# Optimization experiments

Measured on AMD Instinct MI355X. Metric: run time of the kernel, lower is better.

Reference implementation:

```python
import jax, jax.numpy as jnp
import numpy as np

N, LQ, DM = 8, 2500, 256
NH, NL, NP, NZ = 8, 4, 8, 4
DH = DM // NH
SPATIAL = np.array([[64, 176], [32, 88], [16, 44], [8, 22]], dtype=np.int32)
LEN_IN = int((SPATIAL[:, 0] * SPATIAL[:, 1]).sum())


def setup_inputs() -> dict:
    key = jax.random.key(0)
    ks = jax.random.split(key, 10)
    query = jax.random.normal(ks[0], (N, LQ, DM), dtype=jnp.float32)
    query_pos = jax.random.normal(ks[1], (N, LQ, DM), dtype=jnp.float32)
    reference_points = jax.random.uniform(ks[2], (N, LQ, NZ, 2), dtype=jnp.float32)
    input_flatten = jax.random.normal(ks[3], (N, LEN_IN, DM), dtype=jnp.float32)
    input_spatial_shapes = jnp.asarray(SPATIAL)
    lsi = np.concatenate([[0], np.cumsum(SPATIAL[:, 0] * SPATIAL[:, 1])[:-1]]).astype(np.int32)
    input_level_start_index = jnp.asarray(lsi)
    # learned params (Linear: y = x @ W + b, W is (in, out))
    Wv = jax.random.normal(ks[4], (DM, DM), dtype=jnp.float32) * (1.0 / np.sqrt(DM))
    bv = jnp.zeros((DM,), dtype=jnp.float32)
    Wo = jax.random.normal(ks[5], (DM, NH * NL * NP * 2), dtype=jnp.float32) * 0.02
    bo = jax.random.normal(ks[6], (NH * NL * NP * 2,), dtype=jnp.float32) * 1.0
    Wa = jax.random.normal(ks[7], (DM, NH * NL * NP), dtype=jnp.float32) * 0.02
    ba = jnp.zeros((NH * NL * NP,), dtype=jnp.float32)
    return {"query": query, "query_pos": query_pos, "reference_points": reference_points,
            "input_flatten": input_flatten, "input_spatial_shapes": input_spatial_shapes,
            "input_level_start_index": input_level_start_index,
            "Wv": Wv, "bv": bv, "Wo": Wo, "bo": bo, "Wa": Wa, "ba": ba}


def _sample_level(v, h, w, loc):
    """Bilinear sample (grid_sample, align_corners=False, zero padding).
    v:   (N, h*w, NH, DH) level feature map
    loc: (N, Lq, NH, P, 2) normalized locations in [0,1] (x, y)
    returns (N, NH, Lq, P, DH)
    """
    n, hw, nh, dh = v.shape
    lq, p = loc.shape[1], loc.shape[3]
    x = loc[..., 0] * w - 0.5
    y = loc[..., 1] * h - 0.5
    x0f = jnp.floor(x)
    y0f = jnp.floor(y)
    wx = x - x0f
    wy = y - y0f
    x0 = x0f.astype(jnp.int32)
    y0 = y0f.astype(jnp.int32)
    vt = v.transpose(0, 2, 1, 3).reshape(n * nh, hw, dh)

    def gather(xi, yi, wgt):
        valid = ((xi >= 0) & (xi < w) & (yi >= 0) & (yi < h)).astype(v.dtype)
        idx = jnp.clip(yi, 0, h - 1) * w + jnp.clip(xi, 0, w - 1)  # (N,Lq,NH,P)
        idx = idx.transpose(0, 2, 1, 3).reshape(n * nh, lq * p)
        g = jnp.take_along_axis(vt, idx[:, :, None], axis=1)  # (N*NH, Lq*P, DH)
        wv = (wgt * valid).transpose(0, 2, 1, 3).reshape(n * nh, lq * p)
        return g * wv[:, :, None]

    out = (gather(x0, y0, (1 - wx) * (1 - wy))
           + gather(x0 + 1, y0, wx * (1 - wy))
           + gather(x0, y0 + 1, (1 - wx) * wy)
           + gather(x0 + 1, y0 + 1, wx * wy))
    return out.reshape(n, nh, lq, p, dh)


def _forward(query, query_pos, reference_points, input_flatten, spatial, Wv, bv, Wo, bo, Wa, ba):
    n, lq, _ = query.shape
    len_in = input_flatten.shape[1]
    # projections
    value = (input_flatten @ Wv + bv).reshape(n, len_in, NH, DH)
    off = (query @ Wo + bo).reshape(n, lq, NH, NL, NP, 2)
    aw = jax.nn.softmax((query @ Wa + ba).reshape(n, lq, NH, NL * NP), axis=-1)
    aw = aw.reshape(n, lq, NH, NL, NP)
    # normalize offsets by (W_l, H_l), add to Z-anchor reference points
    norm = jnp.asarray(np.stack([spatial[:, 1], spatial[:, 0]], -1), dtype=query.dtype)  # (NL,2)
    off = off / norm[None, None, None, :, None, :]
    off = off.reshape(n, lq, NH, NL, NP // NZ, NZ, 2)
    ref = reference_points[:, :, None, None, None, :, :]  # (N,Lq,1,1,1,NZ,2)
    loc = (ref + off).reshape(n, lq, NH, NL, NP, 2)
    # multi-scale deformable sampling + weighted reduction
    out = jnp.zeros((n, lq, NH, DH), dtype=query.dtype)
    start = 0
    for lvl in range(NL):
        h, w = int(spatial[lvl, 0]), int(spatial[lvl, 1])
        v_l = value[:, start:start + h * w]
        start += h * w
        samp = _sample_level(v_l, h, w, loc[:, :, :, lvl])  # (N,NH,Lq,NP,DH)
        out = out + jnp.einsum('nhqpd,nqhp->nqhd', samp, aw[:, :, :, lvl])
    return out.reshape(n, lq, DM)


def reference(query, query_pos, reference_points, input_flatten, input_spatial_shapes,
              input_level_start_index, Wv, bv, Wo, bo, Wa, ba):
    spatial = np.asarray(jax.device_get(input_spatial_shapes))
    return _forward(query, query_pos, reference_points, input_flatten, spatial,
                    Wv, bv, Wo, bo, Wa, ba)
```

## Files before the change

kernel.cpp:

```cpp
#include <hip/hip_runtime.h>
#include <hip/hip_fp16.h>

#define N_BATCH 8
#define LQ_     2500
#define DM_     256
#define NH_     8
#define NL_     4
#define NP_     8
#define DH_     32
#define LEN_IN_ 14960
#define KDIM    256

__constant__ int c_w[4]     = {176, 88, 44, 22};
__constant__ int c_h[4]     = {64, 32, 16, 8};
__constant__ int c_start[4] = {0, 11264, 14080, 14784};

using bf16x8 = __attribute__((ext_vector_type(8))) short;
using f32x4  = __attribute__((ext_vector_type(4))) float;

static __device__ inline void split_bf16(float v, unsigned short& hi, unsigned short& lo) {
    unsigned int u = __float_as_uint(v);
    hi = (unsigned short)(u >> 16);
    float hif = __uint_as_float(u & 0xFFFF0000u);
    float l = v - hif;
    lo = (unsigned short)(__float_as_uint(l) >> 16);
}

static __device__ inline unsigned short f2bf_rne(float v) {
    unsigned int u = __float_as_uint(v);
    u += 0x7FFFu + ((u >> 16) & 1u);
    return (unsigned short)(u >> 16);
}

__global__ __launch_bounds__(256) void conv_weights(
    const float* __restrict__ Wv, const float* __restrict__ Wo,
    const float* __restrict__ Wa, const float* __restrict__ bo,
    const float* __restrict__ ba,
    unsigned short* __restrict__ Wv_hi, unsigned short* __restrict__ Wv_lo,
    unsigned short* __restrict__ Wc_hi, unsigned short* __restrict__ Wc_lo,
    float* __restrict__ bcomb)
{
    int id = blockIdx.x * 256 + threadIdx.x;
    if (id < 256 * 256) {
        int n = id >> 8, k = id & 255;
        unsigned short h, l;
        split_bf16(Wv[k * 256 + n], h, l);
        Wv_hi[id] = h; Wv_lo[id] = l;
    } else {
        int id2 = id - 65536;
        if (id2 < 768 * 256) {
            int n = id2 >> 8, k = id2 & 255;
            float v = (n < 512) ? Wo[k * 512 + n] : Wa[k * 256 + (n - 512)];
            unsigned short h, l;
            split_bf16(v, h, l);
            Wc_hi[id2] = h; Wc_lo[id2] = l;
        }
    }
    if (id < 768) bcomb[id] = (id < 512) ? bo[id] : ba[id - 512];
}

template <bool BF16_OUT>
__global__ __launch_bounds__(512, 4) void gemm_mfma2(
    const float* __restrict__ A,
    const unsigned short* __restrict__ Bt_hi,
    const unsigned short* __restrict__ Bt_lo,
    const float* __restrict__ bias,
    float* __restrict__ C,
    unsigned short* __restrict__ Cb,
    int M, int N)
{
    __shared__ unsigned short As[128][40];
    __shared__ unsigned short Bh[128][40];
    __shared__ unsigned short Bl[128][40];

    const int tid  = threadIdx.x;
    const int ntn  = N >> 7;
    const int by   = blockIdx.x / ntn;
    const int bx   = blockIdx.x % ntn;
    const int row0 = by << 7, col0 = bx << 7;
    const int lane = tid & 63, wave = tid >> 6;
    const int wrow = (wave & 1) << 6, wcol = (wave >> 1) << 5;
    const int r16  = lane & 15, quad = lane >> 4;

    const int ar0 = tid >> 3;
    const int ac4 = (tid & 7) << 2;
    const int bn  = tid >> 2;
    const int bg  = (tid & 3) << 3;

    float4 pa[2];
    uint4  pbh, pbl;

#pragma unroll
    for (int i = 0; i < 2; ++i) {
        int row = row0 + ar0 + (i << 6);
        pa[i] = (row < M) ? *(const float4*)&A[(size_t)row * KDIM + ac4]
                          : make_float4(0.f, 0.f, 0.f, 0.f);
    }
    {
        size_t goff = (size_t)(col0 + bn) * KDIM + bg;
        pbh = *(const uint4*)&Bt_hi[goff];
        pbl = *(const uint4*)&Bt_lo[goff];
    }

    f32x4 acc[4][2];
#pragma unroll
    for (int i = 0; i < 4; ++i)
#pragma unroll
        for (int j = 0; j < 2; ++j) acc[i][j] = (f32x4){0.f, 0.f, 0.f, 0.f};

#pragma unroll
    for (int kt = 0; kt < KDIM; kt += 32) {
#pragma unroll
        for (int i = 0; i < 2; ++i) {
            int r = ar0 + (i << 6);
            ushort4 hv;
            hv.x = f2bf_rne(pa[i].x);
            hv.y = f2bf_rne(pa[i].y);
            hv.z = f2bf_rne(pa[i].z);
            hv.w = f2bf_rne(pa[i].w);
            *(ushort4*)&As[r][ac4] = hv;
        }
        *(uint4*)&Bh[bn][bg] = pbh;
        *(uint4*)&Bl[bn][bg] = pbl;
        __syncthreads();

        if (kt + 32 < KDIM) {
#pragma unroll
            for (int i = 0; i < 2; ++i) {
                int row = row0 + ar0 + (i << 6);
                pa[i] = (row < M)
                    ? *(const float4*)&A[(size_t)row * KDIM + kt + 32 + ac4]
                    : make_float4(0.f, 0.f, 0.f, 0.f);
            }
            size_t goff = (size_t)(col0 + bn) * KDIM + kt + 32 + bg;
            pbh = *(const uint4*)&Bt_hi[goff];
            pbl = *(const uint4*)&Bt_lo[goff];
        }

        bf16x8 fbh[2], fbl[2], fa[4];
#pragma unroll
        for (int tn = 0; tn < 2; ++tn) {
            int n = wcol + tn * 16 + r16;
            fbh[tn] = *(const bf16x8*)&Bh[n][quad << 3];
            fbl[tn] = *(const bf16x8*)&Bl[n][quad << 3];
        }
#pragma unroll
        for (int tm = 0; tm < 4; ++tm)
            fa[tm] = *(const bf16x8*)&As[wrow + tm * 16 + r16][quad << 3];
#pragma unroll
        for (int tm = 0; tm < 4; ++tm)
#pragma unroll
            for (int tn = 0; tn < 2; ++tn) {
                acc[tm][tn] = __builtin_amdgcn_mfma_f32_16x16x32_bf16(fa[tm], fbl[tn], acc[tm][tn], 0, 0, 0);
                acc[tm][tn] = __builtin_amdgcn_mfma_f32_16x16x32_bf16(fa[tm], fbh[tn], acc[tm][tn], 0, 0, 0);
            }
        __syncthreads();
    }

    float bvs[2];
#pragma unroll
    for (int tn = 0; tn < 2; ++tn) bvs[tn] = bias[col0 + wcol + tn * 16 + r16];
#pragma unroll
    for (int tm = 0; tm < 4; ++tm) {
#pragma unroll
        for (int i = 0; i < 4; ++i) {
            int row = row0 + wrow + tm * 16 + (quad << 2) + i;
            if (row < M) {
                if (!BF16_OUT) {
                    float* crow = C + (size_t)row * N + col0 + wcol + r16;
#pragma unroll
                    for (int tn = 0; tn < 2; ++tn)
                        crow[tn * 16] = acc[tm][tn][i] + bvs[tn];
                } else {
                    int n   = row / LEN_IN_;
                    int pix = row - n * LEN_IN_;
#pragma unroll
                    for (int tn = 0; tn < 2; ++tn) {
                        int col = col0 + wcol + tn * 16 + r16;
                        int h = col >> 5, dh = col & 31;
                        size_t addr = ((size_t)(n * NH_ + h) * LEN_IN_ + pix) * DH_ + dh;
                        Cb[addr] = f2bf_rne(acc[tm][tn][i] + bvs[tn]);
                    }
                }
            }
        }
    }
}

__global__ __launch_bounds__(256) void ms_sample(
    const unsigned short* __restrict__ value,
    const float* __restrict__ comb,
    const float* __restrict__ ref_pts,
    float* __restrict__ out)
{
    __shared__ uint4 s_desc[2048];

    const int bid = blockIdx.x;
    const int tid = threadIdx.x;

    {
        int q = tid >> 5, h = (tid >> 2) & 7, l = tid & 3;
        int nq = bid * 8 + q;
        const float* row = comb + (size_t)nq * 768;

        float4 L0 = *(const float4*)&row[512 + h * 32 + l * 8];
        float4 L1 = *(const float4*)&row[512 + h * 32 + l * 8 + 4];
        float lg[8] = {L0.x, L0.y, L0.z, L0.w, L1.x, L1.y, L1.z, L1.w};
        float m = lg[0];
#pragma unroll
        for (int i = 1; i < 8; ++i) m = fmaxf(m, lg[i]);
        m = fmaxf(m, __shfl_xor(m, 1));
        m = fmaxf(m, __shfl_xor(m, 2));
        float e[8], s = 0.f;
#pragma unroll
        for (int i = 0; i < 8; ++i) { e[i] = __expf(lg[i] - m); s += e[i]; }
        s += __shfl_xor(s, 1);
        s += __shfl_xor(s, 2);
        float inv = 1.f / s;

        float4 R0 = *(const float4*)&ref_pts[(size_t)nq * 8];
        float4 R1 = *(const float4*)&ref_pts[(size_t)nq * 8 + 4];
        float rx[4] = {R0.x, R0.z, R1.x, R1.z};
        float ry[4] = {R0.y, R0.w, R1.y, R1.w};

        float off[16];
#pragma unroll
        for (int i = 0; i < 4; ++i)
            *(float4*)&off[i * 4] = *(const float4*)&row[h * 64 + l * 16 + i * 4];

        float wl = (float)c_w[l], hl = (float)c_h[l];
        int wli = c_w[l], hli = c_h[l], st = c_start[l];
        uint4* dst = &s_desc[((q * 8 + h) * 4 + l) * 8];
#pragma unroll
        for (int p = 0; p < 8; ++p) {
            int z = p & 3;
            float a = e[p] * inv;
            float x = rx[z] * wl + off[p * 2 + 0] - 0.5f;
            float y = ry[z] * hl + off[p * 2 + 1] - 0.5f;
            float x0f = floorf(x), y0f = floorf(y);
            int   x0 = (int)x0f,  y0 = (int)y0f;
            float wx = x - x0f,   wy = y - y0f;
            unsigned short ix[4];
            float wt[4];
#pragma unroll
            for (int j = 0; j < 4; ++j) {
                int xi = x0 + (j & 1);
                int yi = y0 + (j >> 1);
                float w = ((j & 1) ? wx : 1.f - wx) * ((j >> 1) ? wy : 1.f - wy);
                bool valid = (xi >= 0) && (xi < wli) && (yi >= 0) && (yi < hli);
                int xc = min(max(xi, 0), wli - 1);
                int yc = min(max(yi, 0), hli - 1);
                ix[j] = (unsigned short)(st + yc * wli + xc);
                wt[j] = valid ? a * w : 0.f;
            }
            uint4 d;
            d.x = (unsigned int)ix[0] | ((unsigned int)ix[1] << 16);
            d.y = (unsigned int)ix[2] | ((unsigned int)ix[3] << 16);
            __half2 h01 = __floats2half2_rn(wt[0], wt[1]);
            __half2 h23 = __floats2half2_rn(wt[2], wt[3]);
            d.z = *(unsigned int*)&h01;
            d.w = *(unsigned int*)&h23;
            dst[p] = d;
        }
    }
    __syncthreads();

    int q = tid >> 5, h = (tid >> 2) & 7, dhg = tid & 3;
    int nq = bid * 8 + q;
    int n  = nq / LQ_;
    const unsigned short* vb = value
        + ((size_t)(n * NH_ + h) * LEN_IN_) * DH_ + dhg * 8;
    const uint4* desc = &s_desc[(q * 8 + h) * 32];

    float acc[8];
#pragma unroll
    for (int i = 0; i < 8; ++i) acc[i] = 0.f;

#pragma unroll 2
    for (int s = 0; s < 32; ++s) {
        uint4 d = desc[s];
        float2 w01 = __half22float2(*(const __half2*)&d.z);
        float2 w23 = __half22float2(*(const __half2*)&d.w);
        int i0 = d.x & 0xFFFF, i1 = d.x >> 16;
        int i2 = d.y & 0xFFFF, i3 = d.y >> 16;
        uint4 v0 = *(const uint4*)(vb + i0 * DH_);
        uint4 v1 = *(const uint4*)(vb + i1 * DH_);
        uint4 v2 = *(const uint4*)(vb + i2 * DH_);
        uint4 v3 = *(const uint4*)(vb + i3 * DH_);
        const uint4* vv[4] = {&v0, &v1, &v2, &v3};
        float ww[4] = {w01.x, w01.y, w23.x, w23.y};
#pragma unroll
        for (int c = 0; c < 4; ++c) {
            uint4 v = *vv[c];
            float w = ww[c];
            acc[0] = fmaf(__uint_as_float(v.x << 16), w, acc[0]);
            acc[1] = fmaf(__uint_as_float(v.x & 0xFFFF0000u), w, acc[1]);
            acc[2] = fmaf(__uint_as_float(v.y << 16), w, acc[2]);
            acc[3] = fmaf(__uint_as_float(v.y & 0xFFFF0000u), w, acc[3]);
            acc[4] = fmaf(__uint_as_float(v.z << 16), w, acc[4]);
            acc[5] = fmaf(__uint_as_float(v.z & 0xFFFF0000u), w, acc[5]);
            acc[6] = fmaf(__uint_as_float(v.w << 16), w, acc[6]);
            acc[7] = fmaf(__uint_as_float(v.w & 0xFFFF0000u), w, acc[7]);
        }
    }

    float* op = out + (size_t)nq * 256 + h * 32 + dhg * 8;
    *(float4*)&op[0] = make_float4(acc[0], acc[1], acc[2], acc[3]);
    *(float4*)&op[4] = make_float4(acc[4], acc[5], acc[6], acc[7]);
}

extern "C" void kernel_launch(void* const* d_in, const int* in_sizes, int n_in,
                              void* d_out, int out_size, void* d_ws, size_t ws_size,
                              hipStream_t stream)
{
    const float* query         = (const float*)d_in[0];
    const float* ref_pts       = (const float*)d_in[2];
    const float* input_flatten = (const float*)d_in[3];
    const float* Wv            = (const float*)d_in[6];
    const float* bv            = (const float*)d_in[7];
    const float* Wo            = (const float*)d_in[8];
    const float* bo            = (const float*)d_in[9];
    const float* Wa            = (const float*)d_in[10];
    const float* ba            = (const float*)d_in[11];
    float* out = (float*)d_out;

    char* ws = (char*)d_ws;
    size_t o = 0;
    unsigned short* Wv_hi = (unsigned short*)(ws + o); o += 256 * 256 * 2;
    unsigned short* Wv_lo = (unsigned short*)(ws + o); o += 256 * 256 * 2;
    unsigned short* Wc_hi = (unsigned short*)(ws + o); o += 768 * 256 * 2;
    unsigned short* Wc_lo = (unsigned short*)(ws + o); o += 768 * 256 * 2;
    float*          bcomb = (float*)(ws + o);          o += 768 * 4;
    o = (o + 511) & ~(size_t)511;
    unsigned short* value = (unsigned short*)(ws + o); o += (size_t)119680 * 256 * 2;
    o = (o + 511) & ~(size_t)511;
    float* combq = (float*)(ws + o); o += (size_t)20000 * 768 * 4;

    const int MV = N_BATCH * LEN_IN_;
    const int MQ = N_BATCH * LQ_;

    hipLaunchKernelGGL(conv_weights, dim3(1024), dim3(256), 0, stream,
                       Wv, Wo, Wa, bo, ba, Wv_hi, Wv_lo, Wc_hi, Wc_lo, bcomb);
    hipLaunchKernelGGL((gemm_mfma2<true>), dim3((MV / 128) * 2), dim3(512), 0, stream,
                       input_flatten, Wv_hi, Wv_lo, bv, (float*)nullptr, value, MV, 256);
    hipLaunchKernelGGL((gemm_mfma2<false>), dim3(((MQ + 127) / 128) * 6), dim3(512), 0, stream,
                       query, Wc_hi, Wc_lo, bcomb, combq, (unsigned short*)nullptr, MQ, 768);
    hipLaunchKernelGGL(ms_sample, dim3(MQ / 8), dim3(256), 0, stream,
                       value, combq, ref_pts, out);
}
```

Measured before the change: 402.6 us.

## Remap sampler and query GEMM blocks per XCD for value-slice L2 locality

The sampling kernel now assigns each block 64 queries of a single (batch, head) slice, and maps block IDs so that each XCD handles a fixed set of slices. The aim is to keep each slice's bf16 value map resident in that XCD's L2 rather than spread across all of them. The descriptor shared array is padded to 33 to avoid LDS bank conflicts. The combined query GEMM also gets an XCD-aware block swizzle with early exit for padding blocks, at the cost of some idle blocks and a partially filled tail chunk per slice.

```diff
diff --git a/kernel.cpp b/kernel.cpp
--- a/kernel.cpp
+++ b/kernel.cpp
@@ -59,7 +59,7 @@
     if (id < 768) bcomb[id] = (id < 512) ? bo[id] : ba[id - 512];
 }
 
-template <bool BF16_OUT>
+template <bool BF16_OUT, bool XSWIZ>
 __global__ __launch_bounds__(512, 4) void gemm_mfma2(
     const float* __restrict__ A,
     const unsigned short* __restrict__ Bt_hi,
@@ -67,7 +67,7 @@
     const float* __restrict__ bias,
     float* __restrict__ C,
     unsigned short* __restrict__ Cb,
-    int M, int N)
+    int M, int N, int nbm)
 {
     __shared__ unsigned short As[128][40];
     __shared__ unsigned short Bh[128][40];
@@ -75,8 +75,16 @@
 
     const int tid  = threadIdx.x;
     const int ntn  = N >> 7;
-    const int by   = blockIdx.x / ntn;
-    const int bx   = blockIdx.x % ntn;
+    int by, bx;
+    if (XSWIZ) {
+        int xcd = blockIdx.x & 7, j = blockIdx.x >> 3;
+        by = xcd + 8 * (j / ntn);
+        bx = j % ntn;
+        if (by >= nbm) return;
+    } else {
+        by = blockIdx.x / ntn;
+        bx = blockIdx.x % ntn;
+    }
     const int row0 = by << 7, col0 = bx << 7;
     const int lane = tid & 63, wave = tid >> 6;
     const int wrow = (wave & 1) << 6, wcol = (wave >> 1) << 5;
@@ -193,84 +201,92 @@
     const float* __restrict__ ref_pts,
     float* __restrict__ out)
 {
-    __shared__ uint4 s_desc[2048];
-
-    const int bid = blockIdx.x;
-    const int tid = threadIdx.x;
+    __shared__ uint4 s_desc[64][33];
+
+    const int b     = blockIdx.x;
+    const int xcd   = b & 7;
+    const int j     = b >> 3;
+    const int slice = (j / 40) * 8 + xcd;
+    const int chunk = j % 40;
+    const int n     = slice >> 3, h = slice & 7;
+    const int q0    = chunk * 64;
+    const int tid   = threadIdx.x;
 
     {
-        int q = tid >> 5, h = (tid >> 2) & 7, l = tid & 3;
-        int nq = bid * 8 + q;
-        const float* row = comb + (size_t)nq * 768;
-
-        float4 L0 = *(const float4*)&row[512 + h * 32 + l * 8];
-        float4 L1 = *(const float4*)&row[512 + h * 32 + l * 8 + 4];
-        float lg[8] = {L0.x, L0.y, L0.z, L0.w, L1.x, L1.y, L1.z, L1.w};
-        float m = lg[0];
-#pragma unroll
-        for (int i = 1; i < 8; ++i) m = fmaxf(m, lg[i]);
-        m = fmaxf(m, __shfl_xor(m, 1));
-        m = fmaxf(m, __shfl_xor(m, 2));
-        float e[8], s = 0.f;
-#pragma unroll
-        for (int i = 0; i < 8; ++i) { e[i] = __expf(lg[i] - m); s += e[i]; }
-        s += __shfl_xor(s, 1);
-        s += __shfl_xor(s, 2);
-        float inv = 1.f / s;
-
-        float4 R0 = *(const float4*)&ref_pts[(size_t)nq * 8];
-        float4 R1 = *(const float4*)&ref_pts[(size_t)nq * 8 + 4];
-        float rx[4] = {R0.x, R0.z, R1.x, R1.z};
-        float ry[4] = {R0.y, R0.w, R1.y, R1.w};
-
-        float off[16];
-#pragma unroll
-        for (int i = 0; i < 4; ++i)
-            *(float4*)&off[i * 4] = *(const float4*)&row[h * 64 + l * 16 + i * 4];
-
-        float wl = (float)c_w[l], hl = (float)c_h[l];
-        int wli = c_w[l], hli = c_h[l], st = c_start[l];
-        uint4* dst = &s_desc[((q * 8 + h) * 4 + l) * 8];
-#pragma unroll
-        for (int p = 0; p < 8; ++p) {
-            int z = p & 3;
-            float a = e[p] * inv;
-            float x = rx[z] * wl + off[p * 2 + 0] - 0.5f;
-            float y = ry[z] * hl + off[p * 2 + 1] - 0.5f;
-            float x0f = floorf(x), y0f = floorf(y);
-            int   x0 = (int)x0f,  y0 = (int)y0f;
-            float wx = x - x0f,   wy = y - y0f;
-            unsigned short ix[4];
-            float wt[4];
-#pragma unroll
-            for (int j = 0; j < 4; ++j) {
-                int xi = x0 + (j & 1);
-                int yi = y0 + (j >> 1);
-                float w = ((j & 1) ? wx : 1.f - wx) * ((j >> 1) ? wy : 1.f - wy);
-                bool valid = (xi >= 0) && (xi < wli) && (yi >= 0) && (yi < hli);
-                int xc = min(max(xi, 0), wli - 1);
-                int yc = min(max(yi, 0), hli - 1);
-                ix[j] = (unsigned short)(st + yc * wli + xc);
-                wt[j] = valid ? a * w : 0.f;
+        int ql = tid >> 2, l = tid & 3;
+        int q  = q0 + ql;
+        if (q < LQ_) {
+            int nq = n * LQ_ + q;
+            const float* row = comb + (size_t)nq * 768;
+
+            float4 L0 = *(const float4*)&row[512 + h * 32 + l * 8];
+            float4 L1 = *(const float4*)&row[512 + h * 32 + l * 8 + 4];
+            float lg[8] = {L0.x, L0.y, L0.z, L0.w, L1.x, L1.y, L1.z, L1.w};
+            float m = lg[0];
+#pragma unroll
+            for (int i = 1; i < 8; ++i) m = fmaxf(m, lg[i]);
+            m = fmaxf(m, __shfl_xor(m, 1));
+            m = fmaxf(m, __shfl_xor(m, 2));
+            float e[8], s = 0.f;
+#pragma unroll
+            for (int i = 0; i < 8; ++i) { e[i] = __expf(lg[i] - m); s += e[i]; }
+            s += __shfl_xor(s, 1);
+            s += __shfl_xor(s, 2);
+            float inv = 1.f / s;
+
+            float4 R0 = *(const float4*)&ref_pts[(size_t)nq * 8];
+            float4 R1 = *(const float4*)&ref_pts[(size_t)nq * 8 + 4];
+            float rx[4] = {R0.x, R0.z, R1.x, R1.z};
+            float ry[4] = {R0.y, R0.w, R1.y, R1.w};
+
+            float off[16];
+#pragma unroll
+            for (int i = 0; i < 4; ++i)
+                *(float4*)&off[i * 4] = *(const float4*)&row[h * 64 + l * 16 + i * 4];
+
+            float wl = (float)c_w[l], hl = (float)c_h[l];
+            int wli = c_w[l], hli = c_h[l], st = c_start[l];
+#pragma unroll
+            for (int p = 0; p < 8; ++p) {
+                int z = p & 3;
+                float a = e[p] * inv;
+                float x = rx[z] * wl + off[p * 2 + 0] - 0.5f;
+                float y = ry[z] * hl + off[p * 2 + 1] - 0.5f;
+                float x0f = floorf(x), y0f = floorf(y);
+                int   x0 = (int)x0f,  y0 = (int)y0f;
+                float wx = x - x0f,   wy = y - y0f;
+                unsigned short ix[4];
+                float wt[4];
+#pragma unroll
+                for (int jj = 0; jj < 4; ++jj) {
+                    int xi = x0 + (jj & 1);
+                    int yi = y0 + (jj >> 1);
+                    float w = ((jj & 1) ? wx : 1.f - wx) * ((jj >> 1) ? wy : 1.f - wy);
+                    bool valid = (xi >= 0) && (xi < wli) && (yi >= 0) && (yi < hli);
+                    int xc = min(max(xi, 0), wli - 1);
+                    int yc = min(max(yi, 0), hli - 1);
+                    ix[jj] = (unsigned short)(yc * wli + xc);
+                    wt[jj] = valid ? a * w : 0.f;
+                }
+                uint4 d;
+                d.x = (unsigned int)(st + ix[0]) | ((unsigned int)(st + ix[1]) << 16);
+                d.y = (unsigned int)(st + ix[2]) | ((unsigned int)(st + ix[3]) << 16);
+                __half2 h01 = __floats2half2_rn(wt[0], wt[1]);
+                __half2 h23 = __floats2half2_rn(wt[2], wt[3]);
+                d.z = *(unsigned int*)&h01;
+                d.w = *(unsigned int*)&h23;
+                s_desc[ql][l * 8 + p] = d;
             }
-            uint4 d;
-            d.x = (unsigned int)ix[0] | ((unsigned int)ix[1] << 16);
-            d.y = (unsigned int)ix[2] | ((unsigned int)ix[3] << 16);
-            __half2 h01 = __floats2half2_rn(wt[0], wt[1]);
-            __half2 h23 = __floats2half2_rn(wt[2], wt[3]);
-            d.z = *(unsigned int*)&h01;
-            d.w = *(unsigned int*)&h23;
-            dst[p] = d;
         }
     }
     __syncthreads();
 
-    int q = tid >> 5, h = (tid >> 2) & 7, dhg = tid & 3;
-    int nq = bid * 8 + q;
-    int n  = nq / LQ_;
+    int ql = tid >> 2, dhg = tid & 3;
+    int q  = q0 + ql;
+    if (q >= LQ_) return;
+    int nq = n * LQ_ + q;
     const unsigned short* vb = value
         + ((size_t)(n * NH_ + h) * LEN_IN_) * DH_ + dhg * 8;
-    const uint4* desc = &s_desc[(q * 8 + h) * 32];
 
     float acc[8];
 #pragma unroll
@@ -278,7 +294,7 @@
 
 #pragma unroll 2
     for (int s = 0; s < 32; ++s) {
-        uint4 d = desc[s];
+        uint4 d = s_desc[ql][s];
         float2 w01 = __half22float2(*(const __half2*)&d.z);
         float2 w23 = __half22float2(*(const __half2*)&d.w);
         int i0 = d.x & 0xFFFF, i1 = d.x >> 16;
@@ -341,10 +357,10 @@
 
     hipLaunchKernelGGL(conv_weights, dim3(1024), dim3(256), 0, stream,
                        Wv, Wo, Wa, bo, ba, Wv_hi, Wv_lo, Wc_hi, Wc_lo, bcomb);
-    hipLaunchKernelGGL((gemm_mfma2<true>), dim3((MV / 128) * 2), dim3(512), 0, stream,
-                       input_flatten, Wv_hi, Wv_lo, bv, (float*)nullptr, value, MV, 256);
-    hipLaunchKernelGGL((gemm_mfma2<false>), dim3(((MQ + 127) / 128) * 6), dim3(512), 0, stream,
-                       query, Wc_hi, Wc_lo, bcomb, combq, (unsigned short*)nullptr, MQ, 768);
-    hipLaunchKernelGGL(ms_sample, dim3(MQ / 8), dim3(256), 0, stream,
+    hipLaunchKernelGGL((gemm_mfma2<true, false>), dim3((MV / 128) * 2), dim3(512), 0, stream,
+                       input_flatten, Wv_hi, Wv_lo, bv, (float*)nullptr, value, MV, 256, 0);
+    hipLaunchKernelGGL((gemm_mfma2<false, true>), dim3(8 * 20 * 6), dim3(512), 0, stream,
+                       query, Wc_hi, Wc_lo, bcomb, combq, (unsigned short*)nullptr, MQ, 768, 157);
+    hipLaunchKernelGGL(ms_sample, dim3(2560), dim3(256), 0, stream,
                        value, combq, ref_pts, out);
 }
```

Result: faster. 368.4 us (-8.5%).
